# Kernel tuning notes

Measured on AMD Instinct MI355X. Metric: run time of the kernel, lower is better.

The kernel has to match this reference:

```python
import jax, jax.numpy as jnp
import numpy as np

N_ENT = 100000


def setup_inputs() -> dict:
    key = jax.random.key(0)
    ks = jax.random.split(key, 10)
    B, D, O, R, E = 50000, 128, 128, 8, 200000
    return {
        "embeddings": jax.random.normal(ks[0], (N_ENT, D), dtype=jnp.float32),
        "head_e": jax.random.normal(ks[1], (B, D), dtype=jnp.float32),
        "tail_e": jax.random.normal(ks[2], (B, D), dtype=jnp.float32),
        "relation_kernel": jax.random.normal(ks[3], (R, D, O), dtype=jnp.float32),
        "self_kernel": jax.random.normal(ks[4], (D, O), dtype=jnp.float32),
        "edge_val": jax.random.uniform(ks[5], (R, E), dtype=jnp.float32),
        "head_idx": jax.random.randint(ks[6], (B,), 0, N_ENT, dtype=jnp.int32),
        "tail_idx": jax.random.randint(ks[7], (B,), 0, N_ENT, dtype=jnp.int32),
        "edge_src": jax.random.randint(ks[8], (R, E), 0, N_ENT, dtype=jnp.int32),
        "edge_dst": jax.random.randint(ks[9], (R, E), 0, N_ENT, dtype=jnp.int32),
    }


def reference(embeddings, head_e, tail_e, relation_kernel, self_kernel,
              edge_val, head_idx, tail_idx, edge_src, edge_dst):
    # Per-relation SpMM: sum_emb[r, row] = sum_{edges e of r with src=row} val[e] * embeddings[dst[e]]
    def spmm(src, dst, val):
        return jax.ops.segment_sum(embeddings[dst] * val[:, None], src,
                                   num_segments=embeddings.shape[0])
    sum_emb = jax.vmap(spmm)(edge_src, edge_dst, edge_val)  # [R, N, D]

    head_update = jnp.take(sum_emb, head_idx, axis=1)  # [R, B, D]
    tail_update = jnp.take(sum_emb, tail_idx, axis=1)  # [R, B, D]

    head_output = head_e @ self_kernel + jnp.einsum('rbd,rdo->bo', head_update, relation_kernel)
    tail_output = tail_e @ self_kernel + jnp.einsum('rbd,rdo->bo', tail_update, relation_kernel)
    return (jax.nn.sigmoid(head_output), jax.nn.sigmoid(tail_output))
```

## Files before the change

### kernel.cpp

```cpp
#include <hip/hip_runtime.h>
#include <hip/hip_bf16.h>
#include <math.h>

#define N_ENT 100000
#define NB    50000
#define NE    200000
#define RR    8
#define NETOT (RR * NE)
#define NSEG  (RR * N_ENT)

typedef float f32x4  __attribute__((ext_vector_type(4)));
typedef short s16x8  __attribute__((ext_vector_type(8)));

__device__ __forceinline__ void split2(float x, short& h, short& l)
{
    unsigned uh = __float_as_uint(x) & 0xffff0000u;
    h = (short)(uh >> 16);
    float r = x - __uint_as_float(uh);
    l = (short)(__float_as_uint(r) >> 16);
}

__device__ __forceinline__ void glds16(const float* g, float* l)
{
    __builtin_amdgcn_global_load_lds(
        (const __attribute__((address_space(1))) void*)g,
        (__attribute__((address_space(3))) void*)l, 16, 0, 0);
}

__global__ __launch_bounds__(256)
void ktconv_k(const float* __restrict__ rel_k, const float* __restrict__ self_k,
              short* __restrict__ Kth, short* __restrict__ Ktl)
{
    const int r = blockIdx.x;
    const float* src = (r < 8) ? rel_k + (size_t)r * 16384 : self_k;
    short* oh = Kth + (size_t)r * 16384;
    short* ol = Ktl + (size_t)r * 16384;
    for (int i = 0; i < 64; ++i) {
        int ix = i * 256 + threadIdx.x;
        int d = ix >> 7, o = ix & 127;
        short h, l;
        split2(src[ix], h, l);
        oh[o * 128 + d] = h;
        ol[o * 128 + d] = l;
    }
}

template<bool FINAL, bool ACCUM>
__global__ __launch_bounds__(256)
void gemm_mfma_k(const float* __restrict__ X, int xstride,
                 const short* __restrict__ Kth, const short* __restrict__ Ktl,
                 int nkc,
                 const float* __restrict__ Abuf, const int* __restrict__ idx,
                 float* __restrict__ out, int nrows)
{
    __shared__ short Bh[128][136];
    __shared__ short Bl[128][136];

    const int t     = threadIdx.x;
    const int wv    = t >> 6;
    const int lane  = t & 63;
    const int col16 = lane & 15;
    const int g     = lane >> 4;
    const int rowbase = blockIdx.x * 128 + wv * 32;

    f32x4 acc[2][8];
#pragma unroll
    for (int m = 0; m < 2; ++m)
#pragma unroll
        for (int c = 0; c < 8; ++c) acc[m][c] = (f32x4){0.f, 0.f, 0.f, 0.f};

    for (int kc = 0; kc < nkc; ++kc) {
        __syncthreads();
        {
            const s16x8* gh = (const s16x8*)(Kth + (size_t)kc * 16384);
            const s16x8* gl = (const s16x8*)(Ktl + (size_t)kc * 16384);
#pragma unroll
            for (int i = 0; i < 8; ++i) {
                int f = t + i * 256;
                int o = f >> 4, c = f & 15;
                *(s16x8*)&Bh[o][c * 8] = gh[f];
                *(s16x8*)&Bl[o][c * 8] = gl[f];
            }
        }
        __syncthreads();

#pragma unroll
        for (int s = 0; s < 4; ++s) {
            s16x8 ah[2], al[2];
#pragma unroll
            for (int m = 0; m < 2; ++m) {
                int r = rowbase + m * 16 + col16;
                if (r > nrows - 1) r = nrows - 1;
                const float* xp = X + (size_t)r * xstride + kc * 128 + s * 32 + g * 8;
                float4 u0 = *(const float4*)xp;
                float4 u1 = *(const float4*)(xp + 4);
                float u[8] = {u0.x, u0.y, u0.z, u0.w, u1.x, u1.y, u1.z, u1.w};
#pragma unroll
                for (int j = 0; j < 8; ++j) {
                    short h, l; split2(u[j], h, l);
                    ah[m][j] = h; al[m][j] = l;
                }
            }
#pragma unroll
            for (int c = 0; c < 8; ++c) {
                s16x8 bh = *(const s16x8*)&Bh[c * 16 + col16][s * 32 + g * 8];
                s16x8 bl = *(const s16x8*)&Bl[c * 16 + col16][s * 32 + g * 8];
#pragma unroll
                for (int m = 0; m < 2; ++m) {
                    acc[m][c] = __builtin_amdgcn_mfma_f32_16x16x32_bf16(ah[m], bh, acc[m][c], 0, 0, 0);
                    acc[m][c] = __builtin_amdgcn_mfma_f32_16x16x32_bf16(ah[m], bl, acc[m][c], 0, 0, 0);
                    acc[m][c] = __builtin_amdgcn_mfma_f32_16x16x32_bf16(al[m], bh, acc[m][c], 0, 0, 0);
                }
            }
        }
    }

#pragma unroll
    for (int m = 0; m < 2; ++m) {
#pragma unroll
        for (int j = 0; j < 4; ++j) {
            int row = rowbase + m * 16 + g * 4 + j;
            if (row >= nrows) continue;
            float* op = out + (size_t)row * 128;
            if (FINAL) {
                int gi = idx[row];
                const float* Ar = Abuf + (size_t)gi * 128;
#pragma unroll
                for (int c = 0; c < 8; ++c) {
                    int col = c * 16 + col16;
                    float x = acc[m][c][j] + Ar[col];
                    op[col] = 1.f / (1.f + __expf(-x));
                }
            } else if (ACCUM) {
#pragma unroll
                for (int c = 0; c < 8; ++c) {
                    int col = c * 16 + col16;
                    op[col] += acc[m][c][j];
                }
            } else {
#pragma unroll
                for (int c = 0; c < 8; ++c)
                    op[c * 16 + col16] = acc[m][c][j];
            }
        }
    }
}

__global__ __launch_bounds__(256)
void count_k(const int* __restrict__ edge_src, unsigned* __restrict__ cnt,
             unsigned char* __restrict__ rank)
{
    int g = blockIdx.x * 256 + threadIdx.x;
    int r = g / NE;
    int src = edge_src[g];
    unsigned old = atomicAdd(&cnt[r * N_ENT + src], 1u);
    rank[g] = (unsigned char)old;
}

__global__ __launch_bounds__(256)
void scan1_k(const unsigned* __restrict__ cnt, unsigned* __restrict__ offs,
             unsigned* __restrict__ bsum)
{
    __shared__ unsigned s[256];
    const int t = threadIdx.x;
    const int base = blockIdx.x * 1024;
    unsigned v[4], sum = 0;
#pragma unroll
    for (int i = 0; i < 4; ++i) {
        int ix = base + t * 4 + i;
        v[i] = (ix < NSEG) ? cnt[ix] : 0u;
        sum += v[i];
    }
    s[t] = sum; __syncthreads();
    for (int off = 1; off < 256; off <<= 1) {
        unsigned x = (t >= off) ? s[t - off] : 0u;
        __syncthreads();
        s[t] += x;
        __syncthreads();
    }
    unsigned run = s[t] - sum;
#pragma unroll
    for (int i = 0; i < 4; ++i) {
        int ix = base + t * 4 + i;
        if (ix < NSEG) offs[ix] = run;
        run += v[i];
    }
    if (t == 255) bsum[blockIdx.x] = s[255];
}

__global__ __launch_bounds__(256)
void scan2_k(unsigned* __restrict__ bsum, int nb)
{
    __shared__ unsigned s[256];
    __shared__ unsigned carry;
    const int t = threadIdx.x;
    if (t == 0) carry = 0;
    __syncthreads();
    for (int base = 0; base < nb; base += 256) {
        unsigned v = (base + t < nb) ? bsum[base + t] : 0u;
        s[t] = v; __syncthreads();
        for (int off = 1; off < 256; off <<= 1) {
            unsigned x = (t >= off) ? s[t - off] : 0u;
            __syncthreads();
            s[t] += x;
            __syncthreads();
        }
        unsigned tot = s[255];
        unsigned excl = s[t] - v + carry;
        if (base + t < nb) bsum[base + t] = excl;
        __syncthreads();
        if (t == 0) carry += tot;
        __syncthreads();
    }
}

__global__ __launch_bounds__(256)
void scan3_k(unsigned* __restrict__ offs, const unsigned* __restrict__ bsum)
{
    const int base = blockIdx.x * 1024;
    unsigned add = bsum[blockIdx.x];
#pragma unroll
    for (int i = 0; i < 4; ++i) {
        int ix = base + threadIdx.x * 4 + i;
        if (ix < NSEG) offs[ix] += add;
    }
    if (blockIdx.x == 0 && threadIdx.x == 0) offs[NSEG] = NETOT;
}

__global__ __launch_bounds__(256)
void fill_k(const int* __restrict__ edge_src, const int* __restrict__ edge_dst,
            const float* __restrict__ edge_val,
            const unsigned* __restrict__ offs,
            const unsigned char* __restrict__ rank,
            int2* __restrict__ recs)
{
    int g = blockIdx.x * 256 + threadIdx.x;
    int r = g / NE;
    int src = edge_src[g];
    int seg = r * N_ENT + src;
    unsigned pos = offs[seg] + rank[g];
    int2 rec;
    rec.x = edge_dst[g];
    rec.y = __float_as_int(edge_val[g]);
    recs[pos] = rec;
}

__global__ __launch_bounds__(256)
void fuse_k(const unsigned* __restrict__ offs, const int2* __restrict__ recs,
            const float* __restrict__ emb,
            const short* __restrict__ Kth, const short* __restrict__ Ktl,
            float* __restrict__ A)
{
    __shared__ float X[32][132];
    __shared__ float gbuf[4][3072];

    const int t     = threadIdx.x;
    const int wv    = t >> 6;
    const int lane  = t & 63;
    const int col16 = lane & 15;
    const int g     = lane >> 4;
    const int s0    = blockIdx.x * 32;
    const int mrow  = (wv >> 1) * 16;
    const int ccol  = (wv & 1) * 64;

    const int mrel = lane >> 3, mr = lane & 7;
    const size_t seg = (size_t)mrel * N_ENT + (size_t)(s0 + wv * 8 + mr);
    const unsigned o_lo = offs[seg];
    const unsigned o_hi = offs[seg + 1];
    const int n = (int)(o_hi - o_lo);
    int2 rc[4];
#pragma unroll
    for (int p = 0; p < 4; ++p) {
        int ii = (p < n) ? p : (n - 1);
        if (ii < 0) ii = 0;
        unsigned pos = o_lo + (unsigned)ii;
        if (pos > (unsigned)(NETOT - 1)) pos = NETOT - 1;
        rc[p] = recs[pos];
    }

    f32x4 acc[4];
#pragma unroll
    for (int c = 0; c < 4; ++c) acc[c] = (f32x4){0.f, 0.f, 0.f, 0.f};

    for (int j = 0; j < RR; ++j) {
        const int base = j << 3;

        float* gb = &gbuf[wv][0];
#pragma unroll
        for (int i = 0; i < 12; ++i) {
            const int eA = 2 * i,      eB = 2 * i + 1;
            const int rwA = eA / 3,    slA = eA % 3;
            const int rwB = eB / 3,    slB = eB % 3;
            int dA = __shfl(rc[slA].x, base + rwA);
            int dB = __shfl(rc[slB].x, base + rwB);
            int d = (lane < 32) ? dA : dB;
            glds16(emb + (size_t)d * 128 + (lane & 31) * 4, gb + i * 256);
        }
        asm volatile("s_waitcnt vmcnt(0)" ::: "memory");
        __builtin_amdgcn_sched_barrier(0);

        unsigned tailmask = 0;
#pragma unroll
        for (int row = 0; row < 8; ++row) {
            int nn = __shfl(n, base + row);
            float a0 = 0.f, a1 = 0.f;
#pragma unroll
            for (int sl = 0; sl < 3; ++sl) {
                const int e = row * 3 + sl;
                float vv = __uint_as_float((unsigned)__shfl(rc[sl].y, base + row));
                float v = (sl < nn) ? vv : 0.f;
                const float* yp = gb + (e >> 1) * 256 + (e & 1) * 128 + lane * 2;
                a0 = fmaf(v, yp[0], a0);
                a1 = fmaf(v, yp[1], a1);
            }
            if (nn > 3) {
                int d4 = __shfl(rc[3].x, base + row);
                float v4 = __uint_as_float((unsigned)__shfl(rc[3].y, base + row));
                float2 y4 = *(const float2*)(emb + (size_t)d4 * 128 + lane * 2);
                a0 = fmaf(v4, y4.x, a0);
                a1 = fmaf(v4, y4.y, a1);
            }
            *(float2*)&X[wv * 8 + row][lane * 2] = (float2){a0, a1};
            if (nn > 4) tailmask |= (1u << row);
        }

        while (tailmask) {
            int row = __builtin_ctz(tailmask);
            tailmask &= tailmask - 1;
            unsigned aa = __shfl(o_lo, base + row);
            int nn = __shfl(n, base + row);
            float2 xv = *(float2*)&X[wv * 8 + row][lane * 2];
            for (int i2 = 4; i2 < nn; ++i2) {
                int2 rc2 = recs[aa + (unsigned)i2];
                float v = __int_as_float(rc2.y);
                float2 yy = *(const float2*)(emb + (size_t)rc2.x * 128 + lane * 2);
                xv.x = fmaf(v, yy.x, xv.x);
                xv.y = fmaf(v, yy.y, xv.y);
            }
            *(float2*)&X[wv * 8 + row][lane * 2] = xv;
        }

        __syncthreads();

        const short* KH = Kth + (size_t)j * 16384;
        const short* KL = Ktl + (size_t)j * 16384;
#pragma unroll
        for (int s = 0; s < 4; ++s) {
            s16x8 bh[4], bl[4];
#pragma unroll
            for (int c = 0; c < 4; ++c) {
                int oo = ccol + c * 16 + col16;
                int k = s * 32 + g * 8;
                bh[c] = *(const s16x8*)(KH + (size_t)oo * 128 + k);
                bl[c] = *(const s16x8*)(KL + (size_t)oo * 128 + k);
            }
            const float* xp = &X[mrow + col16][s * 32 + g * 8];
            float4 u0 = *(const float4*)xp;
            float4 u1 = *(const float4*)(xp + 4);
            float u[8] = {u0.x, u0.y, u0.z, u0.w, u1.x, u1.y, u1.z, u1.w};
            s16x8 ah, al;
#pragma unroll
            for (int q = 0; q < 8; ++q) {
                short h, l; split2(u[q], h, l);
                ah[q] = h; al[q] = l;
            }
#pragma unroll
            for (int c = 0; c < 4; ++c) {
                acc[c] = __builtin_amdgcn_mfma_f32_16x16x32_bf16(ah, bh[c], acc[c], 0, 0, 0);
                acc[c] = __builtin_amdgcn_mfma_f32_16x16x32_bf16(ah, bl[c], acc[c], 0, 0, 0);
                acc[c] = __builtin_amdgcn_mfma_f32_16x16x32_bf16(al, bh[c], acc[c], 0, 0, 0);
            }
        }
        __syncthreads();
    }

#pragma unroll
    for (int jj = 0; jj < 4; ++jj) {
        int row = s0 + mrow + g * 4 + jj;
        float* op = A + (size_t)row * 128 + ccol;
#pragma unroll
        for (int c = 0; c < 4; ++c)
            op[c * 16 + col16] = acc[c][jj];
    }
}

extern "C" void kernel_launch(void* const* d_in, const int* in_sizes, int n_in,
                              void* d_out, int out_size, void* d_ws, size_t ws_size,
                              hipStream_t stream)
{
    const float* emb      = (const float*)d_in[0];
    const float* head_e   = (const float*)d_in[1];
    const float* tail_e   = (const float*)d_in[2];
    const float* rel_k    = (const float*)d_in[3];
    const float* self_k   = (const float*)d_in[4];
    const float* edge_val = (const float*)d_in[5];
    const int*   head_idx = (const int*)d_in[6];
    const int*   tail_idx = (const int*)d_in[7];
    const int*   edge_src = (const int*)d_in[8];
    const int*   edge_dst = (const int*)d_in[9];
    float* out = (float*)d_out;

    char* p = (char*)d_ws;
    auto take = [&](size_t bytes) -> char* {
        char* q = p; p += (bytes + 255) & ~(size_t)255; return q;
    };
    float*         A    = (float*)take((size_t)N_ENT * 128 * sizeof(float));
    int2*          recs = (int2*)take((size_t)NETOT * sizeof(int2));
    unsigned*      cnt  = (unsigned*)take((size_t)NSEG * sizeof(unsigned));
    unsigned*      offs = (unsigned*)take(((size_t)NSEG + 1) * sizeof(unsigned));
    unsigned*      bsum = (unsigned*)take(1024 * sizeof(unsigned));
    unsigned char* rank = (unsigned char*)take((size_t)NETOT);
    short*         Kth  = (short*)take((size_t)9 * 16384 * sizeof(short));
    short*         Ktl  = (short*)take((size_t)9 * 16384 * sizeof(short));

    const int NB1 = (NSEG + 1023) / 1024;
    dim3 blk(256);

    ktconv_k<<<9, blk, 0, stream>>>(rel_k, self_k, Kth, Ktl);
    hipMemsetAsync(cnt, 0, (size_t)NSEG * sizeof(unsigned), stream);
    count_k<<<NETOT / 256, blk, 0, stream>>>(edge_src, cnt, rank);
    scan1_k<<<NB1, blk, 0, stream>>>(cnt, offs, bsum);
    scan2_k<<<1, blk, 0, stream>>>(bsum, NB1);
    scan3_k<<<NB1, blk, 0, stream>>>(offs, bsum);
    fill_k<<<NETOT / 256, blk, 0, stream>>>(edge_src, edge_dst, edge_val,
                                            offs, rank, recs);

    const int gf = N_ENT / 32;
    fuse_k<<<gf, blk, 0, stream>>>(offs, recs, emb, Kth, Ktl, A);

    const int gb = (NB + 127) / 128;
    gemm_mfma_k<true, false><<<gb, blk, 0, stream>>>(
        head_e, 128, Kth + (size_t)8 * 16384, Ktl + (size_t)8 * 16384, 1,
        A, head_idx, out, NB);
    gemm_mfma_k<true, false><<<gb, blk, 0, stream>>>(
        tail_e, 128, Kth + (size_t)8 * 16384, Ktl + (size_t)8 * 16384, 1,
        A, tail_idx, out + (size_t)NB * 128, NB);
}
```

Baseline: 688.6 us.

## Restructure fused SpMM-GEMM kernel into single-wave blocks of 16 rows

Changes fuse_k from 256-thread blocks covering 32 entities to 64-thread single-wavefront blocks covering 16 entities, with each wave computing all 128 output columns. Block-wide __syncthreads are replaced with LDS waitcnt fences, and the gather prefetch now covers four edges per row in two sub-batches, so the per-row fourth-edge global load is gone. This removes cross-wave barriers and improves load balance across many small blocks. In exchange each wave loads twice as much relation-kernel data per output row and holds more accumulator registers.

```diff
diff --git a/kernel.cpp b/kernel.cpp
--- a/kernel.cpp
+++ b/kernel.cpp
@@ -245,141 +245,141 @@
     recs[pos] = rec;
 }
 
-__global__ __launch_bounds__(256)
+__global__ __launch_bounds__(64)
 void fuse_k(const unsigned* __restrict__ offs, const int2* __restrict__ recs,
             const float* __restrict__ emb,
             const short* __restrict__ Kth, const short* __restrict__ Ktl,
             float* __restrict__ A)
 {
-    __shared__ float X[32][132];
-    __shared__ float gbuf[4][3072];
-
-    const int t     = threadIdx.x;
-    const int wv    = t >> 6;
-    const int lane  = t & 63;
+    __shared__ float X[16][132];
+    __shared__ float gbuf[4096];
+
+    const int lane  = threadIdx.x;
     const int col16 = lane & 15;
     const int g     = lane >> 4;
-    const int s0    = blockIdx.x * 32;
-    const int mrow  = (wv >> 1) * 16;
-    const int ccol  = (wv & 1) * 64;
-
-    const int mrel = lane >> 3, mr = lane & 7;
-    const size_t seg = (size_t)mrel * N_ENT + (size_t)(s0 + wv * 8 + mr);
-    const unsigned o_lo = offs[seg];
-    const unsigned o_hi = offs[seg + 1];
-    const int n = (int)(o_hi - o_lo);
-    int2 rc[4];
-#pragma unroll
-    for (int p = 0; p < 4; ++p) {
-        int ii = (p < n) ? p : (n - 1);
-        if (ii < 0) ii = 0;
-        unsigned pos = o_lo + (unsigned)ii;
-        if (pos > (unsigned)(NETOT - 1)) pos = NETOT - 1;
-        rc[p] = recs[pos];
-    }
-
-    f32x4 acc[4];
-#pragma unroll
-    for (int c = 0; c < 4; ++c) acc[c] = (f32x4){0.f, 0.f, 0.f, 0.f};
-
-    for (int j = 0; j < RR; ++j) {
-        const int base = j << 3;
-
-        float* gb = &gbuf[wv][0];
-#pragma unroll
-        for (int i = 0; i < 12; ++i) {
-            const int eA = 2 * i,      eB = 2 * i + 1;
-            const int rwA = eA / 3,    slA = eA % 3;
-            const int rwB = eB / 3,    slB = eB % 3;
-            int dA = __shfl(rc[slA].x, base + rwA);
-            int dB = __shfl(rc[slB].x, base + rwB);
-            int d = (lane < 32) ? dA : dB;
-            glds16(emb + (size_t)d * 128 + (lane & 31) * 4, gb + i * 256);
-        }
-        asm volatile("s_waitcnt vmcnt(0)" ::: "memory");
-        __builtin_amdgcn_sched_barrier(0);
-
-        unsigned tailmask = 0;
-#pragma unroll
-        for (int row = 0; row < 8; ++row) {
-            int nn = __shfl(n, base + row);
-            float a0 = 0.f, a1 = 0.f;
-#pragma unroll
-            for (int sl = 0; sl < 3; ++sl) {
-                const int e = row * 3 + sl;
-                float vv = __uint_as_float((unsigned)__shfl(rc[sl].y, base + row));
-                float v = (sl < nn) ? vv : 0.f;
-                const float* yp = gb + (e >> 1) * 256 + (e & 1) * 128 + lane * 2;
-                a0 = fmaf(v, yp[0], a0);
-                a1 = fmaf(v, yp[1], a1);
-            }
-            if (nn > 3) {
-                int d4 = __shfl(rc[3].x, base + row);
-                float v4 = __uint_as_float((unsigned)__shfl(rc[3].y, base + row));
-                float2 y4 = *(const float2*)(emb + (size_t)d4 * 128 + lane * 2);
-                a0 = fmaf(v4, y4.x, a0);
-                a1 = fmaf(v4, y4.y, a1);
-            }
-            *(float2*)&X[wv * 8 + row][lane * 2] = (float2){a0, a1};
-            if (nn > 4) tailmask |= (1u << row);
-        }
-
-        while (tailmask) {
-            int row = __builtin_ctz(tailmask);
-            tailmask &= tailmask - 1;
-            unsigned aa = __shfl(o_lo, base + row);
-            int nn = __shfl(n, base + row);
-            float2 xv = *(float2*)&X[wv * 8 + row][lane * 2];
-            for (int i2 = 4; i2 < nn; ++i2) {
-                int2 rc2 = recs[aa + (unsigned)i2];
-                float v = __int_as_float(rc2.y);
-                float2 yy = *(const float2*)(emb + (size_t)rc2.x * 128 + lane * 2);
-                xv.x = fmaf(v, yy.x, xv.x);
-                xv.y = fmaf(v, yy.y, xv.y);
-            }
-            *(float2*)&X[wv * 8 + row][lane * 2] = xv;
-        }
-
-        __syncthreads();
-
-        const short* KH = Kth + (size_t)j * 16384;
-        const short* KL = Ktl + (size_t)j * 16384;
-#pragma unroll
-        for (int s = 0; s < 4; ++s) {
-            s16x8 bh[4], bl[4];
-#pragma unroll
-            for (int c = 0; c < 4; ++c) {
-                int oo = ccol + c * 16 + col16;
-                int k = s * 32 + g * 8;
-                bh[c] = *(const s16x8*)(KH + (size_t)oo * 128 + k);
-                bl[c] = *(const s16x8*)(KL + (size_t)oo * 128 + k);
-            }
-            const float* xp = &X[mrow + col16][s * 32 + g * 8];
-            float4 u0 = *(const float4*)xp;
-            float4 u1 = *(const float4*)(xp + 4);
-            float u[8] = {u0.x, u0.y, u0.z, u0.w, u1.x, u1.y, u1.z, u1.w};
-            s16x8 ah, al;
-#pragma unroll
-            for (int q = 0; q < 8; ++q) {
-                short h, l; split2(u[q], h, l);
-                ah[q] = h; al[q] = l;
-            }
-#pragma unroll
-            for (int c = 0; c < 4; ++c) {
-                acc[c] = __builtin_amdgcn_mfma_f32_16x16x32_bf16(ah, bh[c], acc[c], 0, 0, 0);
-                acc[c] = __builtin_amdgcn_mfma_f32_16x16x32_bf16(ah, bl[c], acc[c], 0, 0, 0);
-                acc[c] = __builtin_amdgcn_mfma_f32_16x16x32_bf16(al, bh[c], acc[c], 0, 0, 0);
-            }
-        }
-        __syncthreads();
+    const int s0    = blockIdx.x * 16;
+
+    unsigned o_lo[2]; int n_[2]; int2 rc[2][4];
+#pragma unroll
+    for (int i = 0; i < 2; ++i) {
+        int c = lane + 64 * i;
+        int rel = c >> 4, row = c & 15;
+        size_t seg = (size_t)rel * N_ENT + (size_t)(s0 + row);
+        unsigned lo = offs[seg];
+        unsigned hi = offs[seg + 1];
+        o_lo[i] = lo; n_[i] = (int)(hi - lo);
+#pragma unroll
+        for (int p = 0; p < 4; ++p) {
+            int ii = (p < n_[i]) ? p : (n_[i] - 1);
+            if (ii < 0) ii = 0;
+            unsigned pos = lo + (unsigned)ii;
+            if (pos > (unsigned)(NETOT - 1)) pos = NETOT - 1;
+            rc[i][p] = recs[pos];
+        }
+    }
+
+    f32x4 acc[8];
+#pragma unroll
+    for (int c = 0; c < 8; ++c) acc[c] = (f32x4){0.f, 0.f, 0.f, 0.f};
+
+#pragma unroll
+    for (int jh = 0; jh < 2; ++jh) {
+        for (int j2 = 0; j2 < 4; ++j2) {
+            const int j = jh * 4 + j2;
+            const int sbase = j2 << 4;
+
+            unsigned tailmask = 0;
+#pragma unroll
+            for (int sb = 0; sb < 2; ++sb) {
+                asm volatile("s_waitcnt lgkmcnt(0)" ::: "memory");
+                __builtin_amdgcn_sched_barrier(0);
+#pragma unroll
+                for (int i = 0; i < 16; ++i) {
+                    const int eA = 2 * i,    eB = 2 * i + 1;
+                    const int lrA = eA >> 2, slA = eA & 3;
+                    const int lrB = eB >> 2, slB = eB & 3;
+                    int dA = __shfl(rc[jh][slA].x, sbase + sb * 8 + lrA);
+                    int dB = __shfl(rc[jh][slB].x, sbase + sb * 8 + lrB);
+                    int d = (lane < 32) ? dA : dB;
+                    glds16(emb + (size_t)d * 128 + (lane & 31) * 4,
+                           &gbuf[i * 256]);
+                }
+                asm volatile("s_waitcnt vmcnt(0)" ::: "memory");
+                __builtin_amdgcn_sched_barrier(0);
+#pragma unroll
+                for (int lr = 0; lr < 8; ++lr) {
+                    const int row = sb * 8 + lr;
+                    int src = sbase + row;
+                    int nn = __shfl(n_[jh], src);
+                    float a0 = 0.f, a1 = 0.f;
+#pragma unroll
+                    for (int sl = 0; sl < 4; ++sl) {
+                        const int e = lr * 4 + sl;
+                        float vv = __uint_as_float((unsigned)__shfl(rc[jh][sl].y, src));
+                        float v = (sl < nn) ? vv : 0.f;
+                        const float* yp = &gbuf[(e >> 1) * 256 + (e & 1) * 128 + lane * 2];
+                        a0 = fmaf(v, yp[0], a0);
+                        a1 = fmaf(v, yp[1], a1);
+                    }
+                    *(float2*)&X[row][lane * 2] = (float2){a0, a1};
+                    if (nn > 4) tailmask |= (1u << row);
+                }
+            }
+
+            while (tailmask) {
+                int row = __builtin_ctz(tailmask);
+                tailmask &= tailmask - 1;
+                int src = sbase + row;
+                unsigned aa = __shfl(o_lo[jh], src);
+                int nn = __shfl(n_[jh], src);
+                float2 xv = *(float2*)&X[row][lane * 2];
+                for (int i2 = 4; i2 < nn; ++i2) {
+                    int2 rc2 = recs[aa + (unsigned)i2];
+                    float v = __int_as_float(rc2.y);
+                    float2 yy = *(const float2*)(emb + (size_t)rc2.x * 128 + lane * 2);
+                    xv.x = fmaf(v, yy.x, xv.x);
+                    xv.y = fmaf(v, yy.y, xv.y);
+                }
+                *(float2*)&X[row][lane * 2] = xv;
+            }
+
+            asm volatile("s_waitcnt lgkmcnt(0)" ::: "memory");
+            __builtin_amdgcn_sched_barrier(0);
+
+            const short* KH = Kth + (size_t)j * 16384;
+            const short* KL = Ktl + (size_t)j * 16384;
+#pragma unroll
+            for (int s = 0; s < 4; ++s) {
+                const float* xp = &X[col16][s * 32 + g * 8];
+                float4 u0 = *(const float4*)xp;
+                float4 u1 = *(const float4*)(xp + 4);
+                float u[8] = {u0.x, u0.y, u0.z, u0.w, u1.x, u1.y, u1.z, u1.w};
+                s16x8 ah, al;
+#pragma unroll
+                for (int q = 0; q < 8; ++q) {
+                    short h, l; split2(u[q], h, l);
+                    ah[q] = h; al[q] = l;
+                }
+                const int k = s * 32 + g * 8;
+#pragma unroll
+                for (int c = 0; c < 8; ++c) {
+                    int oo = c * 16 + col16;
+                    s16x8 bh = *(const s16x8*)(KH + (size_t)oo * 128 + k);
+                    s16x8 bl = *(const s16x8*)(KL + (size_t)oo * 128 + k);
+                    acc[c] = __builtin_amdgcn_mfma_f32_16x16x32_bf16(ah, bh, acc[c], 0, 0, 0);
+                    acc[c] = __builtin_amdgcn_mfma_f32_16x16x32_bf16(ah, bl, acc[c], 0, 0, 0);
+                    acc[c] = __builtin_amdgcn_mfma_f32_16x16x32_bf16(al, bh, acc[c], 0, 0, 0);
+                }
+            }
+        }
     }
 
 #pragma unroll
     for (int jj = 0; jj < 4; ++jj) {
-        int row = s0 + mrow + g * 4 + jj;
-        float* op = A + (size_t)row * 128 + ccol;
-#pragma unroll
-        for (int c = 0; c < 4; ++c)
+        int row = s0 + g * 4 + jj;
+        float* op = A + (size_t)row * 128;
+#pragma unroll
+        for (int c = 0; c < 8; ++c)
             op[c * 16 + col16] = acc[c][jj];
     }
 }
@@ -425,8 +425,8 @@
     fill_k<<<NETOT / 256, blk, 0, stream>>>(edge_src, edge_dst, edge_val,
                                             offs, rank, recs);
 
-    const int gf = N_ENT / 32;
-    fuse_k<<<gf, blk, 0, stream>>>(offs, recs, emb, Kth, Ktl, A);
+    const int gf = N_ENT / 16;
+    fuse_k<<<gf, dim3(64), 0, stream>>>(offs, recs, emb, Kth, Ktl, A);
 
     const int gb = (NB + 127) / 128;
     gemm_mfma_k<true, false><<<gb, blk, 0, stream>>>(
```

Result: no change. 679.6 us (-1.3%).
